# Performance work log

Measured on AMD Instinct MI355X. Metric: run time of the kernel, lower is better.

## Reference

```python
import jax, jax.numpy as jnp
import numpy as np

BS, GS, D, KMAX = 256, 1024, 128, 4
VRANGE = 6.0
NEG = -1e30


def _u(key, shape, fan):
    s = 1.0 / np.sqrt(fan)
    return jax.random.uniform(key, shape, jnp.float32, -s, s)


def _gru(x, hp, Wih, Whh, bih, bhh):
    # torch.nn.GRUCell math
    gi = x @ Wih.T + bih
    gh = hp @ Whh.T + bhh
    ir, iz, inn = jnp.split(gi, 3, axis=-1)
    hr, hz, hn = jnp.split(gh, 3, axis=-1)
    r = jax.nn.sigmoid(ir + hr)
    z = jax.nn.sigmoid(iz + hz)
    n = jnp.tanh(inn + r * hn)
    return (1.0 - z) * n + z * hp


def _gather_h(h, idx):  # h [B,G,D], idx [B,1] -> [B,D]
    B, G, Dd = h.shape
    return jnp.take_along_axis(h, jnp.broadcast_to(idx[:, :, None], (B, 1, Dd)), axis=1)[:, 0]


def setup_inputs() -> dict:
    key = jax.random.key(0)
    ks = jax.random.split(key, 32)
    p = {}
    for i, n in enumerate(["K1", "K2", "K3", "K4", "Q1", "Q2", "Q3", "Q4"]):
        p["W_" + n] = _u(ks[i], (D, D), D)
    p["meta_W1"] = _u(ks[8], (8, 9), 9)
    p["meta_b1"] = _u(ks[9], (8,), 9)
    p["meta_W2"] = _u(ks[10], (2 * D, 8), 8)
    p["meta_b2"] = _u(ks[11], (2 * D,), 8)
    p["init_hidden_W"] = _u(ks[12], (D, D), D)
    p["init_hidden_b"] = _u(ks[13], (D,), D)
    p["init_query"] = _u(ks[14], (D,), D)
    for j, r in enumerate(["rnn1", "rnn2"]):
        p[r + "_Wih"] = _u(ks[15 + 4 * j], (3 * D, D), D)
        p[r + "_Whh"] = _u(ks[16 + 4 * j], (3 * D, D), D)
        p[r + "_bih"] = _u(ks[17 + 4 * j], (3 * D,), D)
        p[r + "_bhh"] = _u(ks[18 + 4 * j], (3 * D,), D)
    inp = dict(
        h=jax.random.normal(ks[24], (BS, GS, D), jnp.float32),
        context2=jax.random.normal(ks[25], (BS, 9), jnp.float32),
        rec=jax.random.randint(ks[26], (BS, GS), 0, GS),
        visited_time=jax.random.randint(ks[27], (BS, GS), 0, GS),
        last_action=jax.random.randint(ks[28], (BS, 1), 0, GS),
        fixed_action=jax.random.randint(ks[29], (BS, KMAX), 0, GS),
        k_max=KMAX,
    )
    inp.update(p)
    return inp


def reference(h, context2, rec, visited_time, last_action, fixed_action, k_max,
              W_K1, W_K2, W_K3, W_K4, W_Q1, W_Q2, W_Q3, W_Q4,
              meta_W1, meta_b1, meta_W2, meta_b2,
              init_hidden_W, init_hidden_b, init_query,
              rnn1_Wih, rnn1_Whh, rnn1_bih, rnn1_bhh,
              rnn2_Wih, rnn2_Whh, rnn2_bih, rnn2_bhh):
    bs, gs, d = h.shape
    # with_feature3: meta_linear(context2) -> [V1, V2]
    hid = jax.nn.relu(context2 @ meta_W1.T + meta_b1)
    lv = hid @ meta_W2.T + meta_b2
    V1, V2 = lv[:, :d], lv[:, d:]
    h_mean = h.mean(1)
    q1 = h_mean @ init_hidden_W.T + init_hidden_b
    q2 = q1
    input_q1 = jnp.broadcast_to(init_query[None, :], (bs, d))
    input_q2 = input_q1
    # K-projections are step-invariant; precompute (same math as in-loop linear_K)
    K1h = h @ W_K1.T
    K2h = h @ W_K2.T
    K3h = h @ W_K3.T
    K4h = h @ W_K4.T
    mask = jnp.zeros((bs, gs), bool)
    stopped = jnp.ones((bs,), bool)
    nola = jnp.full((bs, 1), -1, rec.dtype)  # next_of_last_action
    action_index = jnp.zeros((bs, k_max), rec.dtype)
    kal = jnp.zeros((bs, k_max + 1), rec.dtype)
    kar = jnp.zeros((bs, k_max), rec.dtype)
    ll = jnp.zeros((bs,), h.dtype)
    cols = jnp.arange(gs)[None, :]
    vtt = None
    for i in range(k_max):
        q1 = _gru(input_q1, q1, rnn1_Wih, rnn1_Whh, rnn1_bih, rnn1_bhh)
        q2 = _gru(input_q2, q2, rnn2_Wih, rnn2_Whh, rnn2_bih, rnn2_bhh)
        t1 = jnp.tanh(K1h + (q1 @ W_Q1.T)[:, None, :] + K3h * (q1 @ W_Q3.T)[:, None, :])
        t2 = jnp.tanh(K2h + (q2 @ W_Q2.T)[:, None, :] + K4h * (q2 @ W_Q4.T)[:, None, :])
        result = jnp.einsum('bgd,bd->bg', t1, V1) + jnp.einsum('bgd,bd->bg', t2, V2)
        logits = jnp.tanh(result) * VRANGE
        logits = jnp.where(mask, NEG, logits)
        if i == 0:
            logits = jnp.where(cols == last_action[:, :1], NEG, logits)
        action = fixed_action[:, i:i + 1]
        if i > 0:
            action = jnp.where(stopped[:, None], action_index[:, :1], action)
        logp = jax.nn.log_softmax(logits, axis=-1)
        loss_now = jnp.take_along_axis(logp, action, axis=1)[:, 0]
        ll = ll + (jnp.where(stopped, 0.0, loss_now) if i > 0 else loss_now)
        nona = jnp.take_along_axis(rec, action, axis=1)  # next_of_new_action
        a = action[:, 0]
        action_index = action_index.at[:, i].set(a)
        kal = kal.at[:, i].set(jnp.where(stopped, a, kal[:, i]))
        jprev = (i - 1) % k_max
        kar = kar.at[:, jprev].set(jnp.where(~stopped, a, kar[:, jprev]))
        kal = kal.at[:, i + 1].set(nona[:, 0])
        input_q1 = _gather_h(h, action)
        input_q2 = jnp.where(stopped[:, None], input_q1, _gather_h(h, nola % gs))
        hit = (action == nola)[:, 0]
        stopped = (stopped | hit) if i > 0 else hit
        kal = kal.at[:, i].set(jnp.where(stopped, kal[:, (i - 1) % (k_max + 1)], kal[:, i]))
        kar = kar.at[:, i].set(jnp.where(stopped, kar[:, jprev], kar[:, i]))
        if i == 0:
            vtt = (visited_time - jnp.take_along_axis(visited_time, action, axis=1)) % gs
        vtt_a = jnp.take_along_axis(vtt, action, axis=1)
        mask = vtt <= vtt_a
        if i == 0:
            mask = mask | (vtt > gs - 2)
        mask = jnp.where(stopped[:, None] & (cols == action), False, mask)
        allow = (~stopped) & (nona[:, 0] == action_index[:, 0])
        mask = jnp.where(allow[:, None] & (cols == action_index[:, :1]), False, mask)
        nola = jnp.where(stopped[:, None], jnp.array(-1, rec.dtype), nona)
    kar = kar.at[:, -1].set(jnp.where(~stopped, kal[:, -1], kar[:, -1]))
    action_all = jnp.concatenate([action_index, kal[:, :k_max], kar], axis=-1)
    return action_all, ll
```

## Files before the change

### kernel.cpp

```cpp
#include <hip/hip_runtime.h>
#include <hip/hip_bf16.h>
#include <math.h>

#define GS 1024
#define BSZ 256
#define DD 128
#define NEGV -1e30f

typedef __attribute__((ext_vector_type(8))) short bf16x8_t;
typedef __attribute__((ext_vector_type(4))) float f32x4_t;
typedef __attribute__((ext_vector_type(2))) float f32x2_t;

#define WGRU_OFF_BYTES 131072
#define WQP_OFF_BYTES  524288
#define WIHB_OFF_BYTES 655360
#define F_OFF_BYTES    688128
#define FH_HM   0
#define FI_V    262144
#define FJ_AQB  327680
#define FK_RES  851968
#define F_TOTAL 1900544
#define DESC_OFF_BYTES (F_OFF_BYTES + F_TOTAL * 4)

__device__ __forceinline__ float rtanh(float x) {
    float s = fmaf(x, x, 1.0f);
    return x * __builtin_amdgcn_rsqf(s);
}
__device__ __forceinline__ float tanh2(float x) {
    float e = __expf(x + x);
    return fmaf(-2.0f, __builtin_amdgcn_rcpf(e + 1.0f), 1.0f);
}
__device__ __forceinline__ float sigm2(float x) {
    return __builtin_amdgcn_rcpf(1.0f + __expf(-x));
}
__device__ __forceinline__ unsigned short f2bf(float f) {
    union { float f; unsigned u; } v; v.f = f;
    unsigned u = v.u;
    return (unsigned short)((u + 0x7fffu + ((u >> 16) & 1u)) >> 16);
}
#define MFMA16(a, b, c) __builtin_amdgcn_mfma_f32_16x16x32_bf16((a), (b), (c), 0, 0, 0)

__global__ __launch_bounds__(128) void init_kernel(
    const float* __restrict__ h,
    const float* __restrict__ wk1, const float* __restrict__ wk2,
    const float* __restrict__ wk3, const float* __restrict__ wk4,
    const float* __restrict__ wq1, const float* __restrict__ wq2,
    const float* __restrict__ wq3, const float* __restrict__ wq4,
    const float* __restrict__ ihw,
    const float* __restrict__ r1ih, const float* __restrict__ r1hh,
    const float* __restrict__ r2ih, const float* __restrict__ r2hh,
    unsigned short* __restrict__ wbf, unsigned short* __restrict__ wgru,
    unsigned short* __restrict__ wqp, unsigned short* __restrict__ wihb,
    float* __restrict__ F)
{
    if (blockIdx.x < 2048) {
        int b = blockIdx.x >> 3, seg = blockIdx.x & 7, d = threadIdx.x;
        const float* base = h + ((size_t)(b * GS + seg * 128)) * DD + d;
        float s = 0.0f;
#pragma unroll 8
        for (int r = 0; r < 128; r++) s += base[(size_t)r * DD];
        F[FH_HM + b * 1024 + seg * 128 + d] = s;
        return;
    }
    int tid = (blockIdx.x - 2048) * 128 + threadIdx.x;
    int nth = 128 * 128;
    const float* wks[4]  = {wk1, wk2, wk3, wk4};
    const float* rws[4]  = {r1ih, r1hh, r2ih, r2hh};
    const float* wqs2[4] = {wq1, wq3, wq2, wq4};

    for (int e = tid; e < 65536; e += nth)
        wbf[e] = f2bf(wks[e >> 14][e & 16383]);
    for (int e = tid; e < 196608; e += nth)
        wgru[e] = f2bf(rws[e / 49152][e % 49152]);
    for (int e = tid; e < 65536; e += nth)
        wqp[e] = f2bf(wqs2[e >> 14][e & 16383]);
    for (int e = tid; e < 16384; e += nth)
        wihb[e] = f2bf(ihw[e]);
}

__global__ __launch_bounds__(256) void prep_kernel(
    const float* __restrict__ h, const float* __restrict__ ctx2,
    const int* __restrict__ rec, const int* __restrict__ vt,
    const int* __restrict__ la_, const int* __restrict__ fa,
    const float* __restrict__ mW1, const float* __restrict__ mb1,
    const float* __restrict__ mW2, const float* __restrict__ mb2,
    const float* __restrict__ ihb, const float* __restrict__ iq,
    const float* __restrict__ b1ih, const float* __restrict__ b1hh,
    const float* __restrict__ b2ih, const float* __restrict__ b2hh,
    const unsigned short* __restrict__ wgru, const unsigned short* __restrict__ wqp,
    const unsigned short* __restrict__ wihb,
    float* __restrict__ F, int* __restrict__ DESC, float* __restrict__ out)
{
    int rho = blockIdx.x & 1;
    int b0  = (blockIdx.x >> 1) * 16;
    int t = threadIdx.x;
    int lane = t & 63, w = t >> 6, ml = lane & 15, quad = lane >> 4;

    __shared__ float hm[16][128];
    __shared__ float hid[16][8];
    __shared__ float Xs[16][132], Qs[16][132], Qn[16][132];
    __shared__ int sdesc[16][26];

    const float* bih = rho ? b2ih : b1ih;
    const float* bhh = rho ? b2hh : b1hh;

    {
        int b = t >> 4, dbase = (t & 15) * 8;
#pragma unroll
        for (int e = 0; e < 8; e++) {
            int d = dbase + e;
            float s = 0.0f;
#pragma unroll
            for (int seg = 0; seg < 8; seg++)
                s += F[FH_HM + (b0 + b) * 1024 + seg * 128 + d];
            hm[b][d] = s * (1.0f / 1024.0f);
        }
    }
    if (t < 128) {
        int b = t >> 3, u = t & 7;
        float a = mb1[u];
        for (int k = 0; k < 9; k++) a += mW1[u * 9 + k] * ctx2[(b0 + b) * 9 + k];
        hid[b][u] = a > 0.0f ? a : 0.0f;
    }
    __syncthreads();

    {
        int b = t >> 4, slot = t & 15;
#pragma unroll
        for (int o = 0; o < 16; o++) {
            int idx = slot + 16 * o;
            float a = mb2[idx];
#pragma unroll
            for (int k = 0; k < 8; k++) a += mW2[idx * 8 + k] * hid[b][k];
            F[FI_V + (b0 + b) * 256 + idx] = a;
        }
    }
    if (t < 16) {
        int b = b0 + t;
        int ai[4], kal[5] = {0, 0, 0, 0, 0}, kar[4] = {0, 0, 0, 0};
        int idesc[26];
        int stopped = 1, nola = -1, vt0 = 0;
        for (int i = 0; i < 4; i++) {
            idesc[16 + i] = stopped;
            idesc[22 + i] = nola;
            int action = fa[b * 4 + i];
            if (i > 0 && stopped) action = ai[0];
            int nona = rec[b * GS + action];
            ai[i] = action;
            if (stopped) kal[i] = action;
            int jprev = (i + 3) & 3;
            if (!stopped) kar[jprev] = action;
            kal[i + 1] = nona;
            int hit = (action == nola) ? 1 : 0;
            int st = (i > 0) ? (stopped | hit) : hit;
            if (st) kal[i] = kal[(i + 4) % 5];
            if (st) kar[i] = kar[jprev];
            if (i == 0) vt0 = vt[b * GS + action];
            idesc[0 + i]  = action;
            idesc[4 + i]  = (vt[b * GS + action] - vt0) & (GS - 1);
            idesc[8 + i]  = st;
            idesc[12 + i] = (!st && (nona == ai[0])) ? 1 : 0;
            nola = st ? -1 : nona;
            stopped = st;
        }
        if (!stopped) kar[3] = kal[4];
        idesc[20] = la_[b];
        idesc[21] = vt0;
        int* dd = DESC + b * 32;
        for (int c = 0; c < 26; c++) { dd[c] = idesc[c]; sdesc[t][c] = idesc[c]; }
        float* oa = out + b * 12;
        for (int c = 0; c < 4; c++) {
            oa[c]     = (float)ai[c];
            oa[4 + c] = (float)kal[c];
            oa[8 + c] = (float)kar[c];
        }
    }
    {
        bf16x8_t am[4];
#pragma unroll
        for (int kt = 0; kt < 4; kt++) {
            int k0 = kt * 32 + quad * 8;
            bf16x8_t a;
#pragma unroll
            for (int e = 0; e < 8; e++) a[e] = (short)f2bf(hm[ml][k0 + e]);
            am[kt] = a;
        }
#pragma unroll
        for (int nt2 = 0; nt2 < 2; nt2++) {
            int n = (w * 2 + nt2) * 16 + ml;
            const unsigned short* wb = wihb + (size_t)n * 128 + quad * 8;
            f32x4_t acc = {0.f, 0.f, 0.f, 0.f};
#pragma unroll
            for (int kt = 0; kt < 4; kt++)
                acc = MFMA16(am[kt], *(const bf16x8_t*)(wb + kt * 32), acc);
            float bias = ihb[n];
#pragma unroll
            for (int r_ = 0; r_ < 4; r_++)
                Qs[quad * 4 + r_][n] = acc[r_] + bias;
        }
    }
    __syncthreads();

    int row = t >> 4, d0 = (t & 15) * 8;
    for (int i = 0; i < 4; i++) {
        {
            if (i > 0) {
#pragma unroll
                for (int e = 0; e < 8; e++) Qs[row][d0 + e] = Qn[row][d0 + e];
            }
            const float* xsrc;
            if (i == 0) xsrc = iq + d0;
            else {
                int a = sdesc[row][i - 1];
                int srcrow;
                if (rho == 0) srcrow = a;
                else {
                    int sE = sdesc[row][16 + (i - 1)];
                    int nl = sdesc[row][22 + (i - 1)];
                    srcrow = sE ? a : (nl & (GS - 1));
                }
                xsrc = h + ((size_t)((b0 + row) * GS + srcrow)) * DD + d0;
            }
#pragma unroll
            for (int e = 0; e < 8; e++) Xs[row][d0 + e] = xsrc[e];
        }
        __syncthreads();

        bf16x8_t ax[4], aq[4];
#pragma unroll
        for (int kt = 0; kt < 4; kt++) {
            int k0 = kt * 32 + quad * 8;
            bf16x8_t a, bb;
#pragma unroll
            for (int e = 0; e < 8; e++) {
                a[e]  = (short)f2bf(Xs[ml][k0 + e]);
                bb[e] = (short)f2bf(Qs[ml][k0 + e]);
            }
            ax[kt] = a; aq[kt] = bb;
        }
        f32x4_t gi[3][2], gh[3][2];
#pragma unroll
        for (int gate = 0; gate < 3; gate++)
#pragma unroll
            for (int sub = 0; sub < 2; sub++) {
                int n = gate * 128 + w * 32 + sub * 16 + ml;
                const unsigned short* wi = wgru + ((size_t)((rho * 2 + 0) * 384 + n)) * 128 + quad * 8;
                const unsigned short* wh = wgru + ((size_t)((rho * 2 + 1) * 384 + n)) * 128 + quad * 8;
                f32x4_t ai = {0.f, 0.f, 0.f, 0.f}, ah = {0.f, 0.f, 0.f, 0.f};
#pragma unroll
                for (int kt = 0; kt < 4; kt++) {
                    ai = MFMA16(ax[kt], *(const bf16x8_t*)(wi + kt * 32), ai);
                    ah = MFMA16(aq[kt], *(const bf16x8_t*)(wh + kt * 32), ah);
                }
                gi[gate][sub] = ai; gh[gate][sub] = ah;
            }
#pragma unroll
        for (int sub = 0; sub < 2; sub++) {
            int d = w * 32 + sub * 16 + ml;
            float bir = bih[d], biz = bih[128 + d], bin_ = bih[256 + d];
            float bhr = bhh[d], bhz = bhh[128 + d], bhn = bhh[256 + d];
#pragma unroll
            for (int r_ = 0; r_ < 4; r_++) {
                int brow = quad * 4 + r_;
                float r = sigm2(gi[0][sub][r_] + bir + gh[0][sub][r_] + bhr);
                float z = sigm2(gi[1][sub][r_] + biz + gh[1][sub][r_] + bhz);
                float n = tanh2(gi[2][sub][r_] + bin_ + r * (gh[2][sub][r_] + bhn));
                float qo = Qs[brow][d];
                Qn[brow][d] = fmaf(z, qo - n, n);
            }
        }
        __syncthreads();

        bf16x8_t aqn[4];
#pragma unroll
        for (int kt = 0; kt < 4; kt++) {
            int k0 = kt * 32 + quad * 8;
            bf16x8_t a;
#pragma unroll
            for (int e = 0; e < 8; e++) a[e] = (short)f2bf(Qn[ml][k0 + e]);
            aqn[kt] = a;
        }
#pragma unroll
        for (int nt = 0; nt < 4; nt++) {
            int n = w * 64 + nt * 16 + ml;
            const unsigned short* wq = wqp + ((size_t)(rho * 256 + n)) * 128 + quad * 8;
            f32x4_t acc = {0.f, 0.f, 0.f, 0.f};
#pragma unroll
            for (int kt = 0; kt < 4; kt++)
                acc = MFMA16(aqn[kt], *(const bf16x8_t*)(wq + kt * 32), acc);
            int sel = rho * 2 + (n >> 7);
            int dd2 = n & 127;
#pragma unroll
            for (int r_ = 0; r_ < 4; r_++) {
                int b2 = b0 + quad * 4 + r_;
                F[FJ_AQB + b2 * 2048 + dd2 * 16 + i * 4 + sel] = acc[r_];
            }
        }
        __syncthreads();
    }
}

#define SROW 136
__global__ __launch_bounds__(1024, 4) void score_kernel(
    const float* __restrict__ h, const unsigned short* __restrict__ wbf,
    float* __restrict__ F)
{
    int b = blockIdx.x >> 1, gh = blockIdx.x & 1;
    int t = threadIdx.x;
    int lane = t & 63, w = t >> 6;
    int ml = lane & 15, quad = lane >> 4;
    int hw = w >> 3, ds = w & 7;
    int dg = ds * 16 + ml;

    __shared__ unsigned short stg[2][16 * SROW];
    __shared__ float red[2][64];

    int matA = hw ? 1 : 0;
    int matM = hw ? 3 : 2;
    bf16x8_t bfr[2][4];
#pragma unroll
    for (int kt = 0; kt < 4; kt++) {
        bfr[0][kt] = *(const bf16x8_t*)(wbf + ((size_t)(matA * 128 + dg)) * 128 + kt * 32 + quad * 8);
        bfr[1][kt] = *(const bf16x8_t*)(wbf + ((size_t)(matM * 128 + dg)) * 128 + kt * 32 + quad * 8);
    }
    float V = F[FI_V + b * 256 + hw * 128 + dg];
    f32x2_t Vs = {V, V};
    const float* AQ = F + FJ_AQB + b * 2048 + dg * 16 + hw * 2;
    f32x2_t aA[2], bB[2];
#pragma unroll
    for (int p = 0; p < 2; p++) {
        f32x2_t q0 = *(const f32x2_t*)(AQ + (2 * p) * 4);
        f32x2_t q1 = *(const f32x2_t*)(AQ + (2 * p + 1) * 4);
        aA[p] = (f32x2_t){q0[0], q1[0]};
        bB[p] = (f32x2_t){q0[1], q1[1]};
    }

    int srow = t >> 6;
    int scol = (t & 63) * 2;
    const float* hbase = h + ((size_t)(b * GS + gh * 512 + srow)) * DD + scol;

    if (t < 128) red[t >> 6][t & 63] = 0.0f;

    f32x2_t pre = *(const f32x2_t*)hbase;
    {
        unsigned int pk = (unsigned int)f2bf(pre[0]) | ((unsigned int)f2bf(pre[1]) << 16);
        *(unsigned int*)&stg[0][srow * SROW + scol] = pk;
    }
    __syncthreads();

    for (int tl = 0; tl < 32; tl++) {
        if (tl + 1 < 32)
            pre = *(const f32x2_t*)(hbase + (size_t)(tl + 1) * 16 * DD);

        const unsigned short* sb = stg[tl & 1];
        f32x4_t c[2];
        c[0] = (f32x4_t){0.f, 0.f, 0.f, 0.f};
        c[1] = (f32x4_t){0.f, 0.f, 0.f, 0.f};
#pragma unroll
        for (int kt = 0; kt < 4; kt++) {
            bf16x8_t af = *(const bf16x8_t*)(sb + ml * SROW + kt * 32 + quad * 8);
            c[0] = MFMA16(af, bfr[0][kt], c[0]);
            c[1] = MFMA16(af, bfr[1][kt], c[1]);
        }
        float v[16];
#pragma unroll
        for (int r = 0; r < 4; r++) {
            f32x2_t c0s = {c[0][r], c[0][r]};
            f32x2_t c1s = {c[1][r], c[1][r]};
#pragma unroll
            for (int p = 0; p < 2; p++) {
                f32x2_t y = c0s + aA[p] + c1s * bB[p];
                f32x2_t s = y * y + (f32x2_t){1.0f, 1.0f};
                f32x2_t rr_ = {__builtin_amdgcn_rsqf(s[0]), __builtin_amdgcn_rsqf(s[1])};
                f32x2_t tv = y * rr_ * Vs;
                v[r * 4 + 2 * p]     = tv[0];
                v[r * 4 + 2 * p + 1] = tv[1];
            }
        }
        {
            int bs = ml & 1;
#pragma unroll
            for (int i = 0; i < 8; i++) {
                float lo = v[2 * i], hi = v[2 * i + 1];
                float send = bs ? lo : hi;
                float recv = __shfl_xor(send, 1);
                v[i] = (bs ? hi : lo) + recv;
            }
        }
        {
            int bs = (ml >> 1) & 1;
#pragma unroll
            for (int i = 0; i < 4; i++) {
                float lo = v[2 * i], hi = v[2 * i + 1];
                float send = bs ? lo : hi;
                float recv = __shfl_xor(send, 2);
                v[i] = (bs ? hi : lo) + recv;
            }
        }
        {
            int bs = (ml >> 2) & 1;
#pragma unroll
            for (int i = 0; i < 2; i++) {
                float lo = v[2 * i], hi = v[2 * i + 1];
                float send = bs ? lo : hi;
                float recv = __shfl_xor(send, 4);
                v[i] = (bs ? hi : lo) + recv;
            }
        }
        {
            int bs = (ml >> 3) & 1;
            float lo = v[0], hi = v[1];
            float send = bs ? lo : hi;
            float recv = __shfl_xor(send, 8);
            v[0] = (bs ? hi : lo) + recv;
        }
        atomicAdd(&red[tl & 1][quad * 16 + ml], v[0]);

        if (tl + 1 < 32) {
            unsigned int pk = (unsigned int)f2bf(pre[0]) | ((unsigned int)f2bf(pre[1]) << 16);
            *(unsigned int*)&stg[(tl + 1) & 1][srow * SROW + scol] = pk;
        }
        __syncthreads();
        if (t < 64) {
            int j = t >> 4, gp = t & 15;
            int ridx = (gp >> 2) * 16 + (gp & 3) * 4 + j;
            float val = red[tl & 1][ridx];
            red[tl & 1][ridx] = 0.0f;
            int g = gh * 512 + tl * 16 + gp;
            F[FK_RES + (size_t)b * 4096 + j * 1024 + g] = val;
        }
    }
}

__global__ __launch_bounds__(256) void finalize_kernel(
    const float* __restrict__ F, const int* __restrict__ DESC,
    const int* __restrict__ vt, float* __restrict__ out)
{
    int b = blockIdx.x, t = threadIdx.x;
    const int* dd = DESC + b * 32;
    int act0 = dd[0], la = dd[20], vt0 = dd[21];
    __shared__ float sred[8];
    __shared__ float schosen;
    float ll = 0.0f;

    int vtts[4];
#pragma unroll
    for (int q = 0; q < 4; q++) {
        int g = t + q * 256;
        vtts[q] = (vt[b * GS + g] - vt0) & (GS - 1);
    }

    for (int j = 0; j < 4; j++) {
        int aj = dd[j];
        float lg[4];
#pragma unroll
        for (int q = 0; q < 4; q++) {
            int g = t + q * 256;
            bool neg;
            if (j == 0) {
                neg = (g == la);
            } else {
                int p = j - 1;
                neg = (vtts[q] <= dd[4 + p]) || (p == 0 && vtts[q] > GS - 2);
                if (dd[8 + p] && g == dd[p]) neg = false;
                if (dd[12 + p] && g == act0) neg = false;
            }
            float r = F[FK_RES + (size_t)b * 4096 + j * 1024 + g];
            float vv = neg ? NEGV : 6.0f * rtanh(r);
            lg[q] = vv;
            if (g == aj) schosen = vv;
        }
        float mx = fmaxf(fmaxf(lg[0], lg[1]), fmaxf(lg[2], lg[3]));
#pragma unroll
        for (int o = 1; o < 64; o <<= 1) mx = fmaxf(mx, __shfl_xor(mx, o));
        if ((t & 63) == 0) sred[t >> 6] = mx;
        __syncthreads();
        mx = fmaxf(fmaxf(sred[0], sred[1]), fmaxf(sred[2], sred[3]));
        float sm = 0.0f;
#pragma unroll
        for (int q = 0; q < 4; q++) sm += __expf(lg[q] - mx);
#pragma unroll
        for (int o = 1; o < 64; o <<= 1) sm += __shfl_xor(sm, o);
        if ((t & 63) == 0) sred[4 + (t >> 6)] = sm;
        __syncthreads();
        if (t == 0) {
            float tot = sred[4] + sred[5] + sred[6] + sred[7];
            float lse = mx + logf(tot);
            int gate = (j == 0) || (!dd[16 + j]);
            if (gate) ll += schosen - lse;
        }
        __syncthreads();
    }
    if (t == 0) out[3072 + b] = ll;
}

extern "C" void kernel_launch(void* const* d_in, const int* in_sizes, int n_in,
                              void* d_out, int out_size, void* d_ws, size_t ws_size,
                              hipStream_t stream)
{
    (void)in_sizes; (void)n_in; (void)out_size; (void)ws_size;
    const float* h    = (const float*)d_in[0];
    const float* ctx2 = (const float*)d_in[1];
    const int*   rec  = (const int*)d_in[2];
    const int*   vtm  = (const int*)d_in[3];
    const int*   la   = (const int*)d_in[4];
    const int*   fa   = (const int*)d_in[5];
    const float* wk1 = (const float*)d_in[7];
    const float* wk2 = (const float*)d_in[8];
    const float* wk3 = (const float*)d_in[9];
    const float* wk4 = (const float*)d_in[10];
    const float* wq1 = (const float*)d_in[11];
    const float* wq2 = (const float*)d_in[12];
    const float* wq3 = (const float*)d_in[13];
    const float* wq4 = (const float*)d_in[14];
    const float* mW1 = (const float*)d_in[15];
    const float* mb1 = (const float*)d_in[16];
    const float* mW2 = (const float*)d_in[17];
    const float* mb2 = (const float*)d_in[18];
    const float* ihw = (const float*)d_in[19];
    const float* ihb = (const float*)d_in[20];
    const float* iq  = (const float*)d_in[21];
    const float* r1ih = (const float*)d_in[22];
    const float* r1hh = (const float*)d_in[23];
    const float* b1ih = (const float*)d_in[24];
    const float* b1hh = (const float*)d_in[25];
    const float* r2ih = (const float*)d_in[26];
    const float* r2hh = (const float*)d_in[27];
    const float* b2ih = (const float*)d_in[28];
    const float* b2hh = (const float*)d_in[29];

    unsigned short* wbf  = (unsigned short*)d_ws;
    unsigned short* wgru = (unsigned short*)((char*)d_ws + WGRU_OFF_BYTES);
    unsigned short* wqp  = (unsigned short*)((char*)d_ws + WQP_OFF_BYTES);
    unsigned short* wihb = (unsigned short*)((char*)d_ws + WIHB_OFF_BYTES);
    float* F   = (float*)((char*)d_ws + F_OFF_BYTES);
    int* DESC  = (int*)((char*)d_ws + DESC_OFF_BYTES);
    float* out = (float*)d_out;

    init_kernel<<<dim3(2176), dim3(128), 0, stream>>>(h, wk1, wk2, wk3, wk4,
                                                      wq1, wq2, wq3, wq4, ihw,
                                                      r1ih, r1hh, r2ih, r2hh,
                                                      wbf, wgru, wqp, wihb, F);
    prep_kernel<<<dim3(32), dim3(256), 0, stream>>>(h, ctx2, rec, vtm, la, fa,
                                                    mW1, mb1, mW2, mb2, ihb, iq,
                                                    b1ih, b1hh, b2ih, b2hh,
                                                    wgru, wqp, wihb, F, DESC, out);
    score_kernel<<<dim3(512), dim3(1024), 0, stream>>>(h, wbf, F);
    finalize_kernel<<<dim3(256), dim3(256), 0, stream>>>(F, DESC, vtm, out);
}
```

Baseline: 465.5 us.

## Widen prep kernel to 512 threads and merge score kernel matrix halves per wave

The prep kernel now runs 512 threads. It keeps its operands as bf16 in shared memory, gathers all four GRU input rows up front, and carries the query state in registers with ping-pong buffers, which removes fp32 conversions and several barriers. The score kernel halves its thread count: each wave holds all four key weight matrices in registers and loads h with 16-byte vector loads. The two additive-attention halves are summed in registers before the shuffle reduction. In exchange, register pressure in the score kernel rises and fewer waves are in flight per block.

```diff
diff --git a/kernel.cpp b/kernel.cpp
--- a/kernel.cpp
+++ b/kernel.cpp
@@ -78,7 +78,7 @@
         wihb[e] = f2bf(ihw[e]);
 }
 
-__global__ __launch_bounds__(256) void prep_kernel(
+__global__ __launch_bounds__(512) void prep_kernel(
     const float* __restrict__ h, const float* __restrict__ ctx2,
     const int* __restrict__ rec, const int* __restrict__ vt,
     const int* __restrict__ la_, const int* __restrict__ fa,
@@ -95,26 +95,26 @@
     int b0  = (blockIdx.x >> 1) * 16;
     int t = threadIdx.x;
     int lane = t & 63, w = t >> 6, ml = lane & 15, quad = lane >> 4;
-
-    __shared__ float hm[16][128];
+    int dloc = w * 16 + ml;
+
+    __shared__ __attribute__((aligned(16))) unsigned short hmb[16][136];
+    __shared__ __attribute__((aligned(16))) unsigned short Xall[4][16][136];
+    __shared__ __attribute__((aligned(16))) unsigned short Qb[2][16][136];
     __shared__ float hid[16][8];
-    __shared__ float Xs[16][132], Qs[16][132], Qn[16][132];
     __shared__ int sdesc[16][26];
 
     const float* bih = rho ? b2ih : b1ih;
     const float* bhh = rho ? b2hh : b1hh;
 
-    {
-        int b = t >> 4, dbase = (t & 15) * 8;
-#pragma unroll
-        for (int e = 0; e < 8; e++) {
-            int d = dbase + e;
-            float s = 0.0f;
-#pragma unroll
-            for (int seg = 0; seg < 8; seg++)
-                s += F[FH_HM + (b0 + b) * 1024 + seg * 128 + d];
-            hm[b][d] = s * (1.0f / 1024.0f);
-        }
+#pragma unroll
+    for (int k = 0; k < 4; k++) {
+        int e = t + 512 * k;
+        int b = e >> 7, d = e & 127;
+        float s = 0.0f;
+#pragma unroll
+        for (int seg = 0; seg < 8; seg++)
+            s += F[FH_HM + (b0 + b) * 1024 + seg * 128 + d];
+        hmb[b][d] = f2bf(s * (1.0f / 1024.0f));
     }
     if (t < 128) {
         int b = t >> 3, u = t & 7;
@@ -122,21 +122,9 @@
         for (int k = 0; k < 9; k++) a += mW1[u * 9 + k] * ctx2[(b0 + b) * 9 + k];
         hid[b][u] = a > 0.0f ? a : 0.0f;
     }
-    __syncthreads();
-
-    {
-        int b = t >> 4, slot = t & 15;
-#pragma unroll
-        for (int o = 0; o < 16; o++) {
-            int idx = slot + 16 * o;
-            float a = mb2[idx];
-#pragma unroll
-            for (int k = 0; k < 8; k++) a += mW2[idx * 8 + k] * hid[b][k];
-            F[FI_V + (b0 + b) * 256 + idx] = a;
-        }
-    }
-    if (t < 16) {
-        int b = b0 + t;
+    if (t >= 128 && t < 144) {
+        int tb = t - 128;
+        int b = b0 + tb;
         int ai[4], kal[5] = {0, 0, 0, 0, 0}, kar[4] = {0, 0, 0, 0};
         int idesc[26];
         int stopped = 1, nola = -1, vt0 = 0;
@@ -167,7 +155,7 @@
         idesc[20] = la_[b];
         idesc[21] = vt0;
         int* dd = DESC + b * 32;
-        for (int c = 0; c < 26; c++) { dd[c] = idesc[c]; sdesc[t][c] = idesc[c]; }
+        for (int c = 0; c < 26; c++) { dd[c] = idesc[c]; sdesc[tb][c] = idesc[c]; }
         float* oa = out + b * 12;
         for (int c = 0; c < 4; c++) {
             oa[c]     = (float)ai[c];
@@ -175,133 +163,112 @@
             oa[8 + c] = (float)kar[c];
         }
     }
+    __syncthreads();
+
+#pragma unroll
+    for (int k = 0; k < 8; k++) {
+        int o = t + 512 * k;
+        int b = o >> 8, idx = o & 255;
+        float a = mb2[idx];
+#pragma unroll
+        for (int u = 0; u < 8; u++) a += mW2[idx * 8 + u] * hid[b][u];
+        F[FI_V + (b0 + b) * 256 + idx] = a;
+    }
+    for (int e = t; e < 2048; e += 512) {
+        int row = e >> 7, d = e & 127;
+        Xall[0][row][d] = f2bf(iq[d]);
+    }
+    for (int e = t; e < 6144; e += 512) {
+        int i = (e >> 11) + 1;
+        int b = (e >> 7) & 15, d = e & 127;
+        int a = sdesc[b][i - 1];
+        int srcrow = a;
+        if (rho) {
+            int sE = sdesc[b][16 + (i - 1)];
+            int nl = sdesc[b][22 + (i - 1)];
+            srcrow = sE ? a : (nl & (GS - 1));
+        }
+        Xall[i][b][d] = f2bf(h[((size_t)((b0 + b) * GS + srcrow)) * DD + d]);
+    }
+    float qreg[4];
     {
         bf16x8_t am[4];
 #pragma unroll
+        for (int kt = 0; kt < 4; kt++)
+            am[kt] = *(const bf16x8_t*)&hmb[ml][kt * 32 + quad * 8];
+        const unsigned short* wb = wihb + (size_t)dloc * 128 + quad * 8;
+        f32x4_t acc = {0.f, 0.f, 0.f, 0.f};
+#pragma unroll
+        for (int kt = 0; kt < 4; kt++)
+            acc = MFMA16(am[kt], *(const bf16x8_t*)(wb + kt * 32), acc);
+        float bias = ihb[dloc];
+#pragma unroll
+        for (int r_ = 0; r_ < 4; r_++) {
+            qreg[r_] = acc[r_] + bias;
+            Qb[0][quad * 4 + r_][dloc] = f2bf(qreg[r_]);
+        }
+    }
+    __syncthreads();
+
+    float bir = bih[dloc], biz = bih[128 + dloc], bin_ = bih[256 + dloc];
+    float bhr = bhh[dloc], bhz = bhh[128 + dloc], bhn = bhh[256 + dloc];
+
+    for (int i = 0; i < 4; i++) {
+        int cur = i & 1;
+        bf16x8_t ax[4], aq[4];
+#pragma unroll
         for (int kt = 0; kt < 4; kt++) {
-            int k0 = kt * 32 + quad * 8;
-            bf16x8_t a;
-#pragma unroll
-            for (int e = 0; e < 8; e++) a[e] = (short)f2bf(hm[ml][k0 + e]);
-            am[kt] = a;
-        }
-#pragma unroll
-        for (int nt2 = 0; nt2 < 2; nt2++) {
-            int n = (w * 2 + nt2) * 16 + ml;
-            const unsigned short* wb = wihb + (size_t)n * 128 + quad * 8;
-            f32x4_t acc = {0.f, 0.f, 0.f, 0.f};
-#pragma unroll
-            for (int kt = 0; kt < 4; kt++)
-                acc = MFMA16(am[kt], *(const bf16x8_t*)(wb + kt * 32), acc);
-            float bias = ihb[n];
-#pragma unroll
-            for (int r_ = 0; r_ < 4; r_++)
-                Qs[quad * 4 + r_][n] = acc[r_] + bias;
-        }
-    }
-    __syncthreads();
-
-    int row = t >> 4, d0 = (t & 15) * 8;
-    for (int i = 0; i < 4; i++) {
-        {
-            if (i > 0) {
-#pragma unroll
-                for (int e = 0; e < 8; e++) Qs[row][d0 + e] = Qn[row][d0 + e];
-            }
-            const float* xsrc;
-            if (i == 0) xsrc = iq + d0;
-            else {
-                int a = sdesc[row][i - 1];
-                int srcrow;
-                if (rho == 0) srcrow = a;
-                else {
-                    int sE = sdesc[row][16 + (i - 1)];
-                    int nl = sdesc[row][22 + (i - 1)];
-                    srcrow = sE ? a : (nl & (GS - 1));
-                }
-                xsrc = h + ((size_t)((b0 + row) * GS + srcrow)) * DD + d0;
-            }
-#pragma unroll
-            for (int e = 0; e < 8; e++) Xs[row][d0 + e] = xsrc[e];
+            ax[kt] = *(const bf16x8_t*)&Xall[i][ml][kt * 32 + quad * 8];
+            aq[kt] = *(const bf16x8_t*)&Qb[cur][ml][kt * 32 + quad * 8];
+        }
+        f32x4_t gi[3], gh[3];
+#pragma unroll
+        for (int gate = 0; gate < 3; gate++) {
+            int n = gate * 128 + dloc;
+            const unsigned short* wi = wgru + ((size_t)((rho * 2 + 0) * 384 + n)) * 128 + quad * 8;
+            const unsigned short* wh = wgru + ((size_t)((rho * 2 + 1) * 384 + n)) * 128 + quad * 8;
+            f32x4_t ai = {0.f, 0.f, 0.f, 0.f}, ah = {0.f, 0.f, 0.f, 0.f};
+#pragma unroll
+            for (int kt = 0; kt < 4; kt++) {
+                ai = MFMA16(ax[kt], *(const bf16x8_t*)(wi + kt * 32), ai);
+                ah = MFMA16(aq[kt], *(const bf16x8_t*)(wh + kt * 32), ah);
+            }
+            gi[gate] = ai; gh[gate] = ah;
+        }
+#pragma unroll
+        for (int r_ = 0; r_ < 4; r_++) {
+            float r = sigm2(gi[0][r_] + bir + gh[0][r_] + bhr);
+            float z = sigm2(gi[1][r_] + biz + gh[1][r_] + bhz);
+            float n = tanh2(gi[2][r_] + bin_ + r * (gh[2][r_] + bhn));
+            qreg[r_] = fmaf(z, qreg[r_] - n, n);
+            Qb[cur ^ 1][quad * 4 + r_][dloc] = f2bf(qreg[r_]);
         }
         __syncthreads();
 
-        bf16x8_t ax[4], aq[4];
-#pragma unroll
-        for (int kt = 0; kt < 4; kt++) {
-            int k0 = kt * 32 + quad * 8;
-            bf16x8_t a, bb;
-#pragma unroll
-            for (int e = 0; e < 8; e++) {
-                a[e]  = (short)f2bf(Xs[ml][k0 + e]);
-                bb[e] = (short)f2bf(Qs[ml][k0 + e]);
-            }
-            ax[kt] = a; aq[kt] = bb;
-        }
-        f32x4_t gi[3][2], gh[3][2];
-#pragma unroll
-        for (int gate = 0; gate < 3; gate++)
-#pragma unroll
-            for (int sub = 0; sub < 2; sub++) {
-                int n = gate * 128 + w * 32 + sub * 16 + ml;
-                const unsigned short* wi = wgru + ((size_t)((rho * 2 + 0) * 384 + n)) * 128 + quad * 8;
-                const unsigned short* wh = wgru + ((size_t)((rho * 2 + 1) * 384 + n)) * 128 + quad * 8;
-                f32x4_t ai = {0.f, 0.f, 0.f, 0.f}, ah = {0.f, 0.f, 0.f, 0.f};
-#pragma unroll
-                for (int kt = 0; kt < 4; kt++) {
-                    ai = MFMA16(ax[kt], *(const bf16x8_t*)(wi + kt * 32), ai);
-                    ah = MFMA16(aq[kt], *(const bf16x8_t*)(wh + kt * 32), ah);
-                }
-                gi[gate][sub] = ai; gh[gate][sub] = ah;
-            }
-#pragma unroll
-        for (int sub = 0; sub < 2; sub++) {
-            int d = w * 32 + sub * 16 + ml;
-            float bir = bih[d], biz = bih[128 + d], bin_ = bih[256 + d];
-            float bhr = bhh[d], bhz = bhh[128 + d], bhn = bhh[256 + d];
-#pragma unroll
-            for (int r_ = 0; r_ < 4; r_++) {
-                int brow = quad * 4 + r_;
-                float r = sigm2(gi[0][sub][r_] + bir + gh[0][sub][r_] + bhr);
-                float z = sigm2(gi[1][sub][r_] + biz + gh[1][sub][r_] + bhz);
-                float n = tanh2(gi[2][sub][r_] + bin_ + r * (gh[2][sub][r_] + bhn));
-                float qo = Qs[brow][d];
-                Qn[brow][d] = fmaf(z, qo - n, n);
-            }
-        }
-        __syncthreads();
-
         bf16x8_t aqn[4];
 #pragma unroll
-        for (int kt = 0; kt < 4; kt++) {
-            int k0 = kt * 32 + quad * 8;
-            bf16x8_t a;
-#pragma unroll
-            for (int e = 0; e < 8; e++) a[e] = (short)f2bf(Qn[ml][k0 + e]);
-            aqn[kt] = a;
-        }
-#pragma unroll
-        for (int nt = 0; nt < 4; nt++) {
-            int n = w * 64 + nt * 16 + ml;
-            const unsigned short* wq = wqp + ((size_t)(rho * 256 + n)) * 128 + quad * 8;
+        for (int kt = 0; kt < 4; kt++)
+            aqn[kt] = *(const bf16x8_t*)&Qb[cur ^ 1][ml][kt * 32 + quad * 8];
+#pragma unroll
+        for (int half = 0; half < 2; half++) {
+            int nrow = half * 128 + dloc;
+            const unsigned short* wq = wqp + ((size_t)(rho * 256 + nrow)) * 128 + quad * 8;
             f32x4_t acc = {0.f, 0.f, 0.f, 0.f};
 #pragma unroll
             for (int kt = 0; kt < 4; kt++)
                 acc = MFMA16(aqn[kt], *(const bf16x8_t*)(wq + kt * 32), acc);
-            int sel = rho * 2 + (n >> 7);
-            int dd2 = n & 127;
+            int sel = rho * 2 + half;
 #pragma unroll
             for (int r_ = 0; r_ < 4; r_++) {
                 int b2 = b0 + quad * 4 + r_;
-                F[FJ_AQB + b2 * 2048 + dd2 * 16 + i * 4 + sel] = acc[r_];
-            }
-        }
-        __syncthreads();
+                F[FJ_AQB + b2 * 2048 + dloc * 16 + i * 4 + sel] = acc[r_];
+            }
+        }
     }
 }
 
 #define SROW 136
-__global__ __launch_bounds__(1024, 4) void score_kernel(
+__global__ __launch_bounds__(512, 4) void score_kernel(
     const float* __restrict__ h, const unsigned short* __restrict__ wbf,
     float* __restrict__ F)
 {
@@ -309,72 +276,76 @@
     int t = threadIdx.x;
     int lane = t & 63, w = t >> 6;
     int ml = lane & 15, quad = lane >> 4;
-    int hw = w >> 3, ds = w & 7;
-    int dg = ds * 16 + ml;
-
-    __shared__ unsigned short stg[2][16 * SROW];
+    int dg = w * 16 + ml;
+
+    __shared__ __attribute__((aligned(16))) unsigned short stg[2][16 * SROW];
     __shared__ float red[2][64];
 
-    int matA = hw ? 1 : 0;
-    int matM = hw ? 3 : 2;
-    bf16x8_t bfr[2][4];
-#pragma unroll
-    for (int kt = 0; kt < 4; kt++) {
-        bfr[0][kt] = *(const bf16x8_t*)(wbf + ((size_t)(matA * 128 + dg)) * 128 + kt * 32 + quad * 8);
-        bfr[1][kt] = *(const bf16x8_t*)(wbf + ((size_t)(matM * 128 + dg)) * 128 + kt * 32 + quad * 8);
-    }
-    float V = F[FI_V + b * 256 + hw * 128 + dg];
-    f32x2_t Vs = {V, V};
-    const float* AQ = F + FJ_AQB + b * 2048 + dg * 16 + hw * 2;
-    f32x2_t aA[2], bB[2];
-#pragma unroll
-    for (int p = 0; p < 2; p++) {
-        f32x2_t q0 = *(const f32x2_t*)(AQ + (2 * p) * 4);
-        f32x2_t q1 = *(const f32x2_t*)(AQ + (2 * p + 1) * 4);
-        aA[p] = (f32x2_t){q0[0], q1[0]};
-        bB[p] = (f32x2_t){q0[1], q1[1]};
-    }
-
-    int srow = t >> 6;
-    int scol = (t & 63) * 2;
+    bf16x8_t bfr[4][4];
+#pragma unroll
+    for (int mat = 0; mat < 4; mat++)
+#pragma unroll
+        for (int kt = 0; kt < 4; kt++)
+            bfr[mat][kt] = *(const bf16x8_t*)(wbf + ((size_t)(mat * 128 + dg)) * 128 + kt * 32 + quad * 8);
+#pragma unroll
+    for (int mat = 0; mat < 4; mat++)
+#pragma unroll
+        for (int kt = 0; kt < 4; kt++)
+            asm volatile("" : "+v"(bfr[mat][kt]));
+
+    const float* Vb = F + FI_V + b * 256;
+    f32x2_t VV = {Vb[dg], Vb[128 + dg]};
+    const float* AQ = F + FJ_AQB + b * 2048 + dg * 16;
+    f32x2_t aa[4], bb[4];
+#pragma unroll
+    for (int j = 0; j < 4; j++) {
+        f32x4_t q = *(const f32x4_t*)(AQ + j * 4);
+        aa[j] = (f32x2_t){q[0], q[2]};
+        bb[j] = (f32x2_t){q[1], q[3]};
+    }
+
+    int srow = t >> 5;
+    int scol = (t & 31) * 4;
     const float* hbase = h + ((size_t)(b * GS + gh * 512 + srow)) * DD + scol;
 
     if (t < 128) red[t >> 6][t & 63] = 0.0f;
 
-    f32x2_t pre = *(const f32x2_t*)hbase;
+    f32x4_t pre = *(const f32x4_t*)hbase;
     {
-        unsigned int pk = (unsigned int)f2bf(pre[0]) | ((unsigned int)f2bf(pre[1]) << 16);
-        *(unsigned int*)&stg[0][srow * SROW + scol] = pk;
+        uint2 pk;
+        pk.x = (unsigned)f2bf(pre[0]) | ((unsigned)f2bf(pre[1]) << 16);
+        pk.y = (unsigned)f2bf(pre[2]) | ((unsigned)f2bf(pre[3]) << 16);
+        *(uint2*)&stg[0][srow * SROW + scol] = pk;
     }
     __syncthreads();
 
     for (int tl = 0; tl < 32; tl++) {
         if (tl + 1 < 32)
-            pre = *(const f32x2_t*)(hbase + (size_t)(tl + 1) * 16 * DD);
+            pre = *(const f32x4_t*)(hbase + (size_t)(tl + 1) * 16 * DD);
 
         const unsigned short* sb = stg[tl & 1];
-        f32x4_t c[2];
-        c[0] = (f32x4_t){0.f, 0.f, 0.f, 0.f};
-        c[1] = (f32x4_t){0.f, 0.f, 0.f, 0.f};
+        f32x4_t c[4];
+#pragma unroll
+        for (int mat = 0; mat < 4; mat++) c[mat] = (f32x4_t){0.f, 0.f, 0.f, 0.f};
 #pragma unroll
         for (int kt = 0; kt < 4; kt++) {
             bf16x8_t af = *(const bf16x8_t*)(sb + ml * SROW + kt * 32 + quad * 8);
-            c[0] = MFMA16(af, bfr[0][kt], c[0]);
-            c[1] = MFMA16(af, bfr[1][kt], c[1]);
+#pragma unroll
+            for (int mat = 0; mat < 4; mat++)
+                c[mat] = MFMA16(af, bfr[mat][kt], c[mat]);
         }
         float v[16];
 #pragma unroll
         for (int r = 0; r < 4; r++) {
-            f32x2_t c0s = {c[0][r], c[0][r]};
-            f32x2_t c1s = {c[1][r], c[1][r]};
-#pragma unroll
-            for (int p = 0; p < 2; p++) {
-                f32x2_t y = c0s + aA[p] + c1s * bB[p];
+            f32x2_t cA = {c[0][r], c[1][r]};
+            f32x2_t cM = {c[2][r], c[3][r]};
+#pragma unroll
+            for (int j = 0; j < 4; j++) {
+                f32x2_t y = cA + aa[j] + cM * bb[j];
                 f32x2_t s = y * y + (f32x2_t){1.0f, 1.0f};
-                f32x2_t rr_ = {__builtin_amdgcn_rsqf(s[0]), __builtin_amdgcn_rsqf(s[1])};
-                f32x2_t tv = y * rr_ * Vs;
-                v[r * 4 + 2 * p]     = tv[0];
-                v[r * 4 + 2 * p + 1] = tv[1];
+                f32x2_t rs = {__builtin_amdgcn_rsqf(s[0]), __builtin_amdgcn_rsqf(s[1])};
+                f32x2_t tv = y * rs * VV;
+                v[r * 4 + j] = tv[0] + tv[1];
             }
         }
         {
@@ -417,8 +388,10 @@
         atomicAdd(&red[tl & 1][quad * 16 + ml], v[0]);
 
         if (tl + 1 < 32) {
-            unsigned int pk = (unsigned int)f2bf(pre[0]) | ((unsigned int)f2bf(pre[1]) << 16);
-            *(unsigned int*)&stg[(tl + 1) & 1][srow * SROW + scol] = pk;
+            uint2 pk;
+            pk.x = (unsigned)f2bf(pre[0]) | ((unsigned)f2bf(pre[1]) << 16);
+            pk.y = (unsigned)f2bf(pre[2]) | ((unsigned)f2bf(pre[3]) << 16);
+            *(uint2*)&stg[(tl + 1) & 1][srow * SROW + scol] = pk;
         }
         __syncthreads();
         if (t < 64) {
@@ -541,10 +514,10 @@
                                                       wq1, wq2, wq3, wq4, ihw,
                                                       r1ih, r1hh, r2ih, r2hh,
                                                       wbf, wgru, wqp, wihb, F);
-    prep_kernel<<<dim3(32), dim3(256), 0, stream>>>(h, ctx2, rec, vtm, la, fa,
+    prep_kernel<<<dim3(32), dim3(512), 0, stream>>>(h, ctx2, rec, vtm, la, fa,
                                                     mW1, mb1, mW2, mb2, ihb, iq,
                                                     b1ih, b1hh, b2ih, b2hh,
                                                     wgru, wqp, wihb, F, DESC, out);
-    score_kernel<<<dim3(512), dim3(1024), 0, stream>>>(h, wbf, F);
+    score_kernel<<<dim3(512), dim3(512), 0, stream>>>(h, wbf, F);
     finalize_kernel<<<dim3(256), dim3(256), 0, stream>>>(F, DESC, vtm, out);
 }
```

Result: faster. 404.4 us (-13.1%).
